# Performance work log

Hardware: AMD Instinct MI355X
Metric: run time of the kernel (lower is better)

## Reference

```python
import jax, jax.numpy as jnp
import numpy as np

B, S, D, O, E, K = 4, 1024, 512, 512, 8, 2


def setup_inputs() -> dict:
    key = jax.random.key(0)
    ks = jax.random.split(key, 9)
    sd = 1.0 / np.sqrt(D)
    so = 1.0 / np.sqrt(O)
    return {
        "x": jax.random.normal(ks[0], (B, S, D), dtype=jnp.float32),
        "gate_w": jax.random.uniform(ks[1], (D, E), minval=-sd, maxval=sd, dtype=jnp.float32),
        "gate_b": jax.random.uniform(ks[2], (E,), minval=-sd, maxval=sd, dtype=jnp.float32),
        "w1": jax.random.uniform(ks[3], (E, D, O), minval=-sd, maxval=sd, dtype=jnp.float32),
        "b1": jax.random.uniform(ks[4], (E, O), minval=-sd, maxval=sd, dtype=jnp.float32),
        "w2": jax.random.uniform(ks[5], (E, O, O), minval=-so, maxval=so, dtype=jnp.float32),
        "b2": jax.random.uniform(ks[6], (E, O), minval=-so, maxval=so, dtype=jnp.float32),
        "w3": jax.random.uniform(ks[7], (E, O, O), minval=-so, maxval=so, dtype=jnp.float32),
        "b3": jax.random.uniform(ks[8], (E, O), minval=-so, maxval=so, dtype=jnp.float32),
    }


def reference(x, gate_w, gate_b, w1, b1, w2, b2, w3, b3):
    # Gating: softmax over experts, then top-k expert selection per token.
    logits = jnp.einsum('bsd,de->bse', x, gate_w) + gate_b
    probs = jax.nn.softmax(logits, axis=-1)                 # [B,S,E]
    _, top_idx = jax.lax.top_k(probs, K)                    # [B,S,K]

    n = B * S
    xt = x.reshape(n, D)
    idx_f = top_idx.reshape(n, K)
    # Faithful quirk of the original: the combine weight for slot j is
    # gateProbabilities[b, s, j] (indexing by the SLOT index, not the
    # selected expert id), because nonzero() yields the top-k slot column.
    slot_w = probs.reshape(n, E)[:, :K]                     # [n,K]

    # Dense per-expert 3-layer MLP (grouped GEMM baseline).
    h = jax.nn.relu(jnp.einsum('nd,edh->enh', xt, w1) + b1[:, None, :])
    h = jax.nn.relu(jnp.einsum('enh,eho->eno', h, w2) + b2[:, None, :])
    y = jax.nn.relu(jnp.einsum('enh,eho->eno', h, w3) + b3[:, None, :])  # [E,n,O]

    # combine[n,e] = sum_j 1[top_idx[n,j]==e] * slot_w[n,j]
    combine = jnp.einsum('nke,nk->ne', jax.nn.one_hot(idx_f, E, dtype=xt.dtype), slot_w)
    out = jnp.einsum('ne,eno->no', combine, y)
    return out.reshape(B, S, O)
```

## Files before the change

kernel.cpp:

```cpp
#include <hip/hip_runtime.h>
#include <hip/hip_bf16.h>
#include <float.h>


#define NTOK   4096
#define DIM    512
#define NEXP   8
#define MATSZ  (DIM * DIM)

typedef _Float16 half8 __attribute__((ext_vector_type(8)));
typedef float    f32x4 __attribute__((ext_vector_type(4)));

#define META_OFF   0u
#define TOPE_OFF   1024u
#define TOPW_OFF   33792u
#define ETOK_OFF   66560u
#define EW_OFF     197632u
#define XH_OFF     328704u
#define WT_OFF     4523008u

__device__ __forceinline__ int swz(int row) {
    return ((row & 7) << 3) ^ ((row & 8) << 1);
}

__global__ __launch_bounds__(256)
void gate_kernel(const float* __restrict__ x, const float* __restrict__ gw,
                 const float* __restrict__ gb,
                 int* __restrict__ top_e, float* __restrict__ top_w,
                 _Float16* __restrict__ xh, float* __restrict__ out)
{
    int tid = threadIdx.x;
    int n = blockIdx.x * 4 + (tid >> 6);
    int lane = tid & 63;

    float4 z = {0.f, 0.f, 0.f, 0.f};
    float* op = out + (size_t)n * DIM + lane * 8;
    *(float4*)op = z;
    *(float4*)(op + 4) = z;

    const float* xr = x + (size_t)n * DIM + lane * 8;
    float4 v0 = *(const float4*)xr;
    float4 v1 = *(const float4*)(xr + 4);
    float xv[8] = {v0.x, v0.y, v0.z, v0.w, v1.x, v1.y, v1.z, v1.w};

    half8 h = { (_Float16)xv[0], (_Float16)xv[1], (_Float16)xv[2], (_Float16)xv[3],
                (_Float16)xv[4], (_Float16)xv[5], (_Float16)xv[6], (_Float16)xv[7] };
    *(half8*)(xh + (size_t)n * DIM + lane * 8) = h;

    float p[NEXP];
#pragma unroll
    for (int e = 0; e < NEXP; e++) p[e] = 0.f;
    const float* g = gw + (size_t)lane * 64;
#pragma unroll
    for (int j = 0; j < 8; j++)
#pragma unroll
        for (int e = 0; e < NEXP; e++) p[e] += xv[j] * g[j * 8 + e];
#pragma unroll
    for (int e = 0; e < NEXP; e++) {
        float v = p[e];
        for (int off = 32; off; off >>= 1) v += __shfl_xor(v, off, 64);
        p[e] = v;
    }
    if (lane == 0) {
        float l[NEXP];
#pragma unroll
        for (int e = 0; e < NEXP; e++) l[e] = p[e] + gb[e];
        float m = l[0];
#pragma unroll
        for (int e = 1; e < NEXP; e++) m = fmaxf(m, l[e]);
        float ex[NEXP], s = 0.f;
#pragma unroll
        for (int e = 0; e < NEXP; e++) { ex[e] = expf(l[e] - m); s += ex[e]; }
        int e0 = 0; float m0 = l[0];
#pragma unroll
        for (int e = 1; e < NEXP; e++) if (l[e] > m0) { m0 = l[e]; e0 = e; }
        int e1 = -1; float m1 = -FLT_MAX;
#pragma unroll
        for (int e = 0; e < NEXP; e++) if (e != e0 && l[e] > m1) { m1 = l[e]; e1 = e; }
        float inv = 1.f / s;
        top_e[2 * n + 0] = e0;
        top_e[2 * n + 1] = e1;
        top_w[2 * n + 0] = ex[0] * inv;
        top_w[2 * n + 1] = ex[1] * inv;
    }
}

__global__ __launch_bounds__(256)
void scatter_kernel(const int* __restrict__ top_e, const float* __restrict__ top_w,
                    int* __restrict__ meta, int* __restrict__ entry_tok,
                    float* __restrict__ entry_w)
{
    int n = blockIdx.x * 256 + threadIdx.x;
    int lane = threadIdx.x & 63;
#pragma unroll
    for (int j = 0; j < 2; j++) {
        int e = top_e[2 * n + j];
        float ww = top_w[2 * n + j];
        int pos = 0;
        for (int ex = 0; ex < NEXP; ex++) {
            unsigned long long m = __ballot(e == ex);
            if (e == ex) {
                int leader = __ffsll(m) - 1;
                int base = 0;
                if (lane == leader) base = atomicAdd(&meta[8 + ex], __popcll(m));
                base = __shfl(base, leader, 64);
                pos = (ex << 12) + base + __popcll(m & ((1ull << lane) - 1ull));
            }
        }
        entry_tok[pos] = n;
        entry_w[pos] = ww;
    }
}

__global__ __launch_bounds__(256)
void pack_w(const float* __restrict__ W1, const float* __restrict__ W2,
            const float* __restrict__ W3, _Float16* __restrict__ Wt)
{
    __shared__ float s[32 * 513];
    int bid = blockIdx.x;
    int mat = bid >> 4, kc = bid & 15;
    const float* src = ((mat < 8) ? W1 + (size_t)mat * MATSZ
                      : (mat < 16) ? W2 + (size_t)(mat - 8) * MATSZ
                                   : W3 + (size_t)(mat - 16) * MATSZ)
                     + (size_t)kc * 32 * DIM;
    int tid = threadIdx.x;
#pragma unroll
    for (int i = 0; i < 16; i++) {
        int idx = i * 1024 + tid * 4;
        int k = idx >> 9, c = idx & 511;
        float4 v = *(const float4*)(src + idx);
        float* d = &s[k * 513 + c];
        d[0] = v.x; d[1] = v.y; d[2] = v.z; d[3] = v.w;
    }
    __syncthreads();
    int w = tid >> 6, lane = tid & 63, l15 = lane & 15, l4 = lane >> 4;
#pragma unroll
    for (int i = 0; i < 8; i++) {
        int c16 = w * 8 + i;
        int col = c16 * 16 + l15;
        half8 h;
#pragma unroll
        for (int j = 0; j < 8; j++)
            h[j] = (_Float16)s[(l4 * 8 + j) * 513 + col];
        *(half8*)(Wt + (size_t)mat * MATSZ + (size_t)(kc * 32 + c16) * 512 + lane * 8) = h;
    }
}

__global__ __launch_bounds__(512, 2)
void fused_mlp(const _Float16* __restrict__ xh, const _Float16* __restrict__ wt,
               const float* __restrict__ b1, const float* __restrict__ b2,
               const float* __restrict__ b3, float* __restrict__ out,
               const int* __restrict__ meta, const int* __restrict__ entry_tok,
               const float* __restrict__ entry_w)
{
    __shared__ _Float16 hbuf[64 * DIM];
    __shared__ int   rtok[64];
    __shared__ float rw[64];

    int bid = blockIdx.x;
    int e = bid & 7;
    int j = bid >> 3;
    int cnt = meta[8 + e];
    if (j >= ((cnt + 63) >> 6)) return;
    int row0 = (e << 12) + (j << 6);

    int tid = threadIdx.x;
    int w = tid >> 6, l = tid & 63;
    int l15 = l & 15, l4 = l >> 4;
    int colb = w * 64 + l15;

    if (tid < 64) {
        int t = entry_tok[row0 + tid];
        rtok[tid] = t;
        rw[tid]   = entry_w[row0 + tid];
    }
    __syncthreads();

    {
        int row = tid >> 3;
        int c0 = (tid & 7) * 64;
        int tk = rtok[row]; if (tk < 0) tk = 0;
        const _Float16* src = xh + (size_t)tk * DIM + c0;
        int f = swz(row);
        _Float16* dst = hbuf + row * DIM;
#pragma unroll
        for (int q = 0; q < 8; q++) {
            half8 v = *(const half8*)(src + q * 8);
            *(half8*)(dst + ((c0 + q * 8) ^ f)) = v;
        }
    }
    __syncthreads();

    f32x4 acc[4][4];

    auto run_layer = [&](const _Float16* __restrict__ Wp) {
#pragma unroll
        for (int rg = 0; rg < 4; rg++)
#pragma unroll
            for (int cg = 0; cg < 4; cg++) acc[rg][cg] = (f32x4){0.f, 0.f, 0.f, 0.f};
        const _Float16* wb = Wp + (size_t)(w * 4) * 512 + (size_t)l * 8;
        half8 b[2][4];
#pragma unroll
        for (int cg = 0; cg < 4; cg++)
            b[0][cg] = *(const half8*)(wb + (size_t)cg * 512);
#pragma unroll
        for (int kc = 0; kc < 16; kc++) {
            const int cur = kc & 1, nxt = cur ^ 1;
            const int kn = (kc + 1) & 15;
#pragma unroll
            for (int cg = 0; cg < 4; cg++)
                b[nxt][cg] = *(const half8*)(wb + (size_t)(kn * 32 + cg) * 512);
            int koff = kc * 32 + l4 * 8;
            half8 af[4];
#pragma unroll
            for (int rg = 0; rg < 4; rg++) {
                int row = rg * 16 + l15;
                af[rg] = *(const half8*)(hbuf + row * DIM + (koff ^ swz(row)));
            }
#pragma unroll
            for (int rg = 0; rg < 4; rg++)
#pragma unroll
                for (int cg = 0; cg < 4; cg++)
                    acc[rg][cg] = __builtin_amdgcn_mfma_f32_16x16x32_f16(af[rg], b[cur][cg], acc[rg][cg], 0, 0, 0);
        }
    };

    auto writeback = [&](const float* __restrict__ Bias) {
        float bs[4];
#pragma unroll
        for (int cg = 0; cg < 4; cg++) bs[cg] = Bias[e * DIM + colb + cg * 16];
        __syncthreads();
#pragma unroll
        for (int rg = 0; rg < 4; rg++)
#pragma unroll
            for (int r = 0; r < 4; r++) {
                int row = rg * 16 + l4 * 4 + r;
                int f = swz(row);
                _Float16* dst = hbuf + row * DIM;
#pragma unroll
                for (int cg = 0; cg < 4; cg++)
                    dst[(colb + cg * 16) ^ f] = (_Float16)fmaxf(acc[rg][cg][r] + bs[cg], 0.f);
            }
        __syncthreads();
    };

    run_layer(wt + (size_t)e * MATSZ);        writeback(b1);
    run_layer(wt + (size_t)(8 + e) * MATSZ);  writeback(b2);
    run_layer(wt + (size_t)(16 + e) * MATSZ);

    float bs[4];
#pragma unroll
    for (int cg = 0; cg < 4; cg++) bs[cg] = b3[e * DIM + colb + cg * 16];
#pragma unroll
    for (int rg = 0; rg < 4; rg++)
#pragma unroll
        for (int r = 0; r < 4; r++) {
            int row = rg * 16 + l4 * 4 + r;
            int tok = rtok[row];
            if (tok >= 0) {
                float ww = rw[row];
                float* op = out + (size_t)tok * DIM + colb;
#pragma unroll
                for (int cg = 0; cg < 4; cg++) {
                    float v = fmaxf(acc[rg][cg][r] + bs[cg], 0.f);
                    atomicAdd(op + cg * 16, ww * v);
                }
            }
        }
}

extern "C" void kernel_launch(void* const* d_in, const int* in_sizes, int n_in,
                              void* d_out, int out_size, void* d_ws, size_t ws_size,
                              hipStream_t stream)
{
    const float* x      = (const float*)d_in[0];
    const float* gate_w = (const float*)d_in[1];
    const float* gate_b = (const float*)d_in[2];
    const float* w1     = (const float*)d_in[3];
    const float* b1     = (const float*)d_in[4];
    const float* w2     = (const float*)d_in[5];
    const float* b2     = (const float*)d_in[6];
    const float* w3     = (const float*)d_in[7];
    const float* b3     = (const float*)d_in[8];
    float* out = (float*)d_out;

    char* ws = (char*)d_ws;
    int*      meta      = (int*)(ws + META_OFF);
    int*      top_e     = (int*)(ws + TOPE_OFF);
    float*    top_w     = (float*)(ws + TOPW_OFF);
    int*      entry_tok = (int*)(ws + ETOK_OFF);
    float*    entry_w   = (float*)(ws + EW_OFF);
    _Float16* xh        = (_Float16*)(ws + XH_OFF);
    _Float16* wt        = (_Float16*)(ws + WT_OFF);

    hipMemsetAsync(meta, 0, 256, stream);

    gate_kernel<<<NTOK / 4, 256, 0, stream>>>(x, gate_w, gate_b, top_e, top_w, xh, out);
    scatter_kernel<<<NTOK / 256, 256, 0, stream>>>(top_e, top_w, meta, entry_tok, entry_w);
    pack_w<<<24 * 16, 256, 0, stream>>>(w1, w2, w3, wt);

    fused_mlp<<<NEXP * 64, 512, 0, stream>>>(xh, wt, b1, b2, b3, out,
                                             meta, entry_tok, entry_w);
}
```

Measured before the change: 158.5 us.

## Replace atomic combine with slot buffer plus gather kernel, merge gate and weight pack

Merges the weight-pack and gating kernels into one launch. Rewrites scatter to use block-local shared-memory counters and padded global counters, and records each token's slot positions. The MLP kernel now writes unweighted expert outputs to a slot buffer instead of doing float atomicAdds into the output, and a new combine kernel gathers and weights the two slots per token. The B-fragment prefetch is deepened to three buffers and the MFMA block is wrapped in raised wave priority. This adds an extra kernel and an intermediate buffer round trip in exchange for removing atomics and the output zeroing.

```diff
diff --git a/kernel.cpp b/kernel.cpp
--- a/kernel.cpp
+++ b/kernel.cpp
@@ -14,29 +14,59 @@
 #define META_OFF   0u
 #define TOPE_OFF   1024u
 #define TOPW_OFF   33792u
-#define ETOK_OFF   66560u
-#define EW_OFF     197632u
-#define XH_OFF     328704u
-#define WT_OFF     4523008u
+#define INV_OFF    66560u
+#define ETOK_OFF   99328u
+#define XH_OFF     230400u
+#define WT_OFF     4424704u
+#define Y_OFF      17007616u
 
 __device__ __forceinline__ int swz(int row) {
     return ((row & 7) << 3) ^ ((row & 8) << 1);
 }
 
 __global__ __launch_bounds__(256)
-void gate_kernel(const float* __restrict__ x, const float* __restrict__ gw,
+void prep_kernel(const float* __restrict__ x, const float* __restrict__ gw,
                  const float* __restrict__ gb,
+                 const float* __restrict__ W1, const float* __restrict__ W2,
+                 const float* __restrict__ W3,
                  int* __restrict__ top_e, float* __restrict__ top_w,
-                 _Float16* __restrict__ xh, float* __restrict__ out)
-{
+                 _Float16* __restrict__ xh, _Float16* __restrict__ Wt)
+{
+    __shared__ float s[32 * 513];
+    int bid = blockIdx.x;
     int tid = threadIdx.x;
-    int n = blockIdx.x * 4 + (tid >> 6);
+
+    if (bid < 384) {
+        int mat = bid >> 4, kc = bid & 15;
+        const float* src = ((mat < 8) ? W1 + (size_t)mat * MATSZ
+                          : (mat < 16) ? W2 + (size_t)(mat - 8) * MATSZ
+                                       : W3 + (size_t)(mat - 16) * MATSZ)
+                         + (size_t)kc * 32 * DIM;
+#pragma unroll
+        for (int i = 0; i < 16; i++) {
+            int idx = i * 1024 + tid * 4;
+            int k = idx >> 9, c = idx & 511;
+            float4 v = *(const float4*)(src + idx);
+            float* d = &s[k * 513 + c];
+            d[0] = v.x; d[1] = v.y; d[2] = v.z; d[3] = v.w;
+        }
+        __syncthreads();
+        int w = tid >> 6, lane = tid & 63, l15 = lane & 15, l4 = lane >> 4;
+#pragma unroll
+        for (int i = 0; i < 8; i++) {
+            int c16 = w * 8 + i;
+            int col = c16 * 16 + l15;
+            half8 h;
+#pragma unroll
+            for (int j = 0; j < 8; j++)
+                h[j] = (_Float16)s[(l4 * 8 + j) * 513 + col];
+            *(half8*)(Wt + (size_t)mat * MATSZ + (size_t)(kc * 32 + c16) * 512 + lane * 8) = h;
+        }
+        return;
+    }
+
+    int n = (bid - 384) * 4 + (tid >> 6);
     int lane = tid & 63;
-
-    float4 z = {0.f, 0.f, 0.f, 0.f};
-    float* op = out + (size_t)n * DIM + lane * 8;
-    *(float4*)op = z;
-    *(float4*)(op + 4) = z;
 
     const float* xr = x + (size_t)n * DIM + lane * 8;
     float4 v0 = *(const float4*)xr;
@@ -68,99 +98,63 @@
         float m = l[0];
 #pragma unroll
         for (int e = 1; e < NEXP; e++) m = fmaxf(m, l[e]);
-        float ex[NEXP], s = 0.f;
-#pragma unroll
-        for (int e = 0; e < NEXP; e++) { ex[e] = expf(l[e] - m); s += ex[e]; }
+        float ex[NEXP], sum = 0.f;
+#pragma unroll
+        for (int e = 0; e < NEXP; e++) { ex[e] = expf(l[e] - m); sum += ex[e]; }
         int e0 = 0; float m0 = l[0];
 #pragma unroll
         for (int e = 1; e < NEXP; e++) if (l[e] > m0) { m0 = l[e]; e0 = e; }
         int e1 = -1; float m1 = -FLT_MAX;
 #pragma unroll
         for (int e = 0; e < NEXP; e++) if (e != e0 && l[e] > m1) { m1 = l[e]; e1 = e; }
-        float inv = 1.f / s;
-        top_e[2 * n + 0] = e0;
-        top_e[2 * n + 1] = e1;
-        top_w[2 * n + 0] = ex[0] * inv;
-        top_w[2 * n + 1] = ex[1] * inv;
+        float inv = 1.f / sum;
+        int2 te = {e0, e1};
+        *(int2*)(top_e + 2 * n) = te;
+        float2 tw = {ex[0] * inv, ex[1] * inv};
+        *(float2*)(top_w + 2 * n) = tw;
     }
 }
 
 __global__ __launch_bounds__(256)
-void scatter_kernel(const int* __restrict__ top_e, const float* __restrict__ top_w,
-                    int* __restrict__ meta, int* __restrict__ entry_tok,
-                    float* __restrict__ entry_w)
-{
-    int n = blockIdx.x * 256 + threadIdx.x;
-    int lane = threadIdx.x & 63;
-#pragma unroll
-    for (int j = 0; j < 2; j++) {
-        int e = top_e[2 * n + j];
-        float ww = top_w[2 * n + j];
-        int pos = 0;
-        for (int ex = 0; ex < NEXP; ex++) {
-            unsigned long long m = __ballot(e == ex);
-            if (e == ex) {
-                int leader = __ffsll(m) - 1;
-                int base = 0;
-                if (lane == leader) base = atomicAdd(&meta[8 + ex], __popcll(m));
-                base = __shfl(base, leader, 64);
-                pos = (ex << 12) + base + __popcll(m & ((1ull << lane) - 1ull));
-            }
-        }
-        entry_tok[pos] = n;
-        entry_w[pos] = ww;
-    }
-}
-
-__global__ __launch_bounds__(256)
-void pack_w(const float* __restrict__ W1, const float* __restrict__ W2,
-            const float* __restrict__ W3, _Float16* __restrict__ Wt)
-{
-    __shared__ float s[32 * 513];
-    int bid = blockIdx.x;
-    int mat = bid >> 4, kc = bid & 15;
-    const float* src = ((mat < 8) ? W1 + (size_t)mat * MATSZ
-                      : (mat < 16) ? W2 + (size_t)(mat - 8) * MATSZ
-                                   : W3 + (size_t)(mat - 16) * MATSZ)
-                     + (size_t)kc * 32 * DIM;
+void scatter_kernel(const int* __restrict__ top_e, int* __restrict__ meta,
+                    int* __restrict__ entry_tok, int* __restrict__ inv_pos)
+{
+    __shared__ int lcnt[NEXP];
+    __shared__ int lbase[NEXP];
     int tid = threadIdx.x;
-#pragma unroll
-    for (int i = 0; i < 16; i++) {
-        int idx = i * 1024 + tid * 4;
-        int k = idx >> 9, c = idx & 511;
-        float4 v = *(const float4*)(src + idx);
-        float* d = &s[k * 513 + c];
-        d[0] = v.x; d[1] = v.y; d[2] = v.z; d[3] = v.w;
-    }
-    __syncthreads();
-    int w = tid >> 6, lane = tid & 63, l15 = lane & 15, l4 = lane >> 4;
-#pragma unroll
-    for (int i = 0; i < 8; i++) {
-        int c16 = w * 8 + i;
-        int col = c16 * 16 + l15;
-        half8 h;
-#pragma unroll
-        for (int j = 0; j < 8; j++)
-            h[j] = (_Float16)s[(l4 * 8 + j) * 513 + col];
-        *(half8*)(Wt + (size_t)mat * MATSZ + (size_t)(kc * 32 + c16) * 512 + lane * 8) = h;
-    }
+    if (tid < NEXP) lcnt[tid] = 0;
+    __syncthreads();
+
+    int n = blockIdx.x * 256 + tid;
+    int2 ee = *(const int2*)(top_e + 2 * n);
+    int r0 = atomicAdd(&lcnt[ee.x], 1);
+    int r1 = atomicAdd(&lcnt[ee.y], 1);
+    __syncthreads();
+
+    if (tid < NEXP) lbase[tid] = atomicAdd(&meta[tid * 16], lcnt[tid]);
+    __syncthreads();
+
+    int p0 = (ee.x << 12) + lbase[ee.x] + r0;
+    int p1 = (ee.y << 12) + lbase[ee.y] + r1;
+    entry_tok[p0] = n;
+    entry_tok[p1] = n;
+    int2 pp = {p0, p1};
+    *(int2*)(inv_pos + 2 * n) = pp;
 }
 
 __global__ __launch_bounds__(512, 2)
 void fused_mlp(const _Float16* __restrict__ xh, const _Float16* __restrict__ wt,
                const float* __restrict__ b1, const float* __restrict__ b2,
-               const float* __restrict__ b3, float* __restrict__ out,
-               const int* __restrict__ meta, const int* __restrict__ entry_tok,
-               const float* __restrict__ entry_w)
+               const float* __restrict__ b3, float* __restrict__ y,
+               const int* __restrict__ meta, const int* __restrict__ entry_tok)
 {
     __shared__ _Float16 hbuf[64 * DIM];
-    __shared__ int   rtok[64];
-    __shared__ float rw[64];
+    __shared__ int rtok[64];
 
     int bid = blockIdx.x;
     int e = bid & 7;
     int j = bid >> 3;
-    int cnt = meta[8 + e];
+    int cnt = meta[e * 16];
     if (j >= ((cnt + 63) >> 6)) return;
     int row0 = (e << 12) + (j << 6);
 
@@ -169,11 +163,8 @@
     int l15 = l & 15, l4 = l >> 4;
     int colb = w * 64 + l15;
 
-    if (tid < 64) {
-        int t = entry_tok[row0 + tid];
-        rtok[tid] = t;
-        rw[tid]   = entry_w[row0 + tid];
-    }
+    if (tid < 64)
+        rtok[tid] = entry_tok[row0 + tid];
     __syncthreads();
 
     {
@@ -199,17 +190,20 @@
 #pragma unroll
             for (int cg = 0; cg < 4; cg++) acc[rg][cg] = (f32x4){0.f, 0.f, 0.f, 0.f};
         const _Float16* wb = Wp + (size_t)(w * 4) * 512 + (size_t)l * 8;
-        half8 b[2][4];
-#pragma unroll
-        for (int cg = 0; cg < 4; cg++)
-            b[0][cg] = *(const half8*)(wb + (size_t)cg * 512);
+        half8 b[3][4];
+#pragma unroll
+        for (int cg = 0; cg < 4; cg++) {
+            b[0][cg] = *(const half8*)(wb + (size_t)(0 * 32 + cg) * 512);
+            b[1][cg] = *(const half8*)(wb + (size_t)(1 * 32 + cg) * 512);
+        }
 #pragma unroll
         for (int kc = 0; kc < 16; kc++) {
-            const int cur = kc & 1, nxt = cur ^ 1;
-            const int kn = (kc + 1) & 15;
+            const int cur = kc % 3;
+            const int pf  = (kc + 2) % 3;
+            const int kn  = (kc + 2) & 15;
 #pragma unroll
             for (int cg = 0; cg < 4; cg++)
-                b[nxt][cg] = *(const half8*)(wb + (size_t)(kn * 32 + cg) * 512);
+                b[pf][cg] = *(const half8*)(wb + (size_t)(kn * 32 + cg) * 512);
             int koff = kc * 32 + l4 * 8;
             half8 af[4];
 #pragma unroll
@@ -217,11 +211,13 @@
                 int row = rg * 16 + l15;
                 af[rg] = *(const half8*)(hbuf + row * DIM + (koff ^ swz(row)));
             }
+            __builtin_amdgcn_s_setprio(1);
 #pragma unroll
             for (int rg = 0; rg < 4; rg++)
 #pragma unroll
                 for (int cg = 0; cg < 4; cg++)
                     acc[rg][cg] = __builtin_amdgcn_mfma_f32_16x16x32_f16(af[rg], b[cur][cg], acc[rg][cg], 0, 0, 0);
+            __builtin_amdgcn_s_setprio(0);
         }
     };
 
@@ -251,22 +247,46 @@
     float bs[4];
 #pragma unroll
     for (int cg = 0; cg < 4; cg++) bs[cg] = b3[e * DIM + colb + cg * 16];
+    float* yb = y + (size_t)row0 * DIM;
 #pragma unroll
     for (int rg = 0; rg < 4; rg++)
 #pragma unroll
         for (int r = 0; r < 4; r++) {
             int row = rg * 16 + l4 * 4 + r;
-            int tok = rtok[row];
-            if (tok >= 0) {
-                float ww = rw[row];
-                float* op = out + (size_t)tok * DIM + colb;
-#pragma unroll
-                for (int cg = 0; cg < 4; cg++) {
-                    float v = fmaxf(acc[rg][cg][r] + bs[cg], 0.f);
-                    atomicAdd(op + cg * 16, ww * v);
-                }
-            }
-        }
+            float* yp = yb + (size_t)row * DIM + colb;
+#pragma unroll
+            for (int cg = 0; cg < 4; cg++)
+                yp[cg * 16] = fmaxf(acc[rg][cg][r] + bs[cg], 0.f);
+        }
+}
+
+__global__ __launch_bounds__(256)
+void combine_kernel(const float* __restrict__ y, const int* __restrict__ inv_pos,
+                    const float* __restrict__ top_w, float* __restrict__ out)
+{
+    int tid = threadIdx.x;
+    int n = blockIdx.x * 4 + (tid >> 6);
+    int lane = tid & 63;
+    int2 pp = *(const int2*)(inv_pos + 2 * n);
+    float2 tw = *(const float2*)(top_w + 2 * n);
+    const float* y0 = y + (size_t)pp.x * DIM + lane * 8;
+    const float* y1 = y + (size_t)pp.y * DIM + lane * 8;
+    float4 a0 = *(const float4*)y0;
+    float4 a1 = *(const float4*)(y0 + 4);
+    float4 c0 = *(const float4*)y1;
+    float4 c1 = *(const float4*)(y1 + 4);
+    float4 o0, o1;
+    o0.x = tw.x * a0.x + tw.y * c0.x;
+    o0.y = tw.x * a0.y + tw.y * c0.y;
+    o0.z = tw.x * a0.z + tw.y * c0.z;
+    o0.w = tw.x * a0.w + tw.y * c0.w;
+    o1.x = tw.x * a1.x + tw.y * c1.x;
+    o1.y = tw.x * a1.y + tw.y * c1.y;
+    o1.z = tw.x * a1.z + tw.y * c1.z;
+    o1.w = tw.x * a1.w + tw.y * c1.w;
+    float* op = out + (size_t)n * DIM + lane * 8;
+    *(float4*)op = o0;
+    *(float4*)(op + 4) = o1;
 }
 
 extern "C" void kernel_launch(void* const* d_in, const int* in_sizes, int n_in,
@@ -288,17 +308,18 @@
     int*      meta      = (int*)(ws + META_OFF);
     int*      top_e     = (int*)(ws + TOPE_OFF);
     float*    top_w     = (float*)(ws + TOPW_OFF);
+    int*      inv_pos   = (int*)(ws + INV_OFF);
     int*      entry_tok = (int*)(ws + ETOK_OFF);
-    float*    entry_w   = (float*)(ws + EW_OFF);
     _Float16* xh        = (_Float16*)(ws + XH_OFF);
     _Float16* wt        = (_Float16*)(ws + WT_OFF);
-
-    hipMemsetAsync(meta, 0, 256, stream);
-
-    gate_kernel<<<NTOK / 4, 256, 0, stream>>>(x, gate_w, gate_b, top_e, top_w, xh, out);
-    scatter_kernel<<<NTOK / 256, 256, 0, stream>>>(top_e, top_w, meta, entry_tok, entry_w);
-    pack_w<<<24 * 16, 256, 0, stream>>>(w1, w2, w3, wt);
-
-    fused_mlp<<<NEXP * 64, 512, 0, stream>>>(xh, wt, b1, b2, b3, out,
-                                             meta, entry_tok, entry_w);
-}
+    float*    yslot     = (float*)(ws + Y_OFF);
+
+    hipMemsetAsync(meta, 0, 1024, stream);
+
+    prep_kernel<<<384 + NTOK / 4, 256, 0, stream>>>(x, gate_w, gate_b, w1, w2, w3,
+                                                    top_e, top_w, xh, wt);
+    scatter_kernel<<<NTOK / 256, 256, 0, stream>>>(top_e, meta, entry_tok, inv_pos);
+    fused_mlp<<<NEXP * 64, 512, 0, stream>>>(xh, wt, b1, b2, b3, yslot,
+                                             meta, entry_tok);
+    combine_kernel<<<NTOK / 4, 256, 0, stream>>>(yslot, inv_pos, top_w, out);
+}
```

Measured after the change: 135.5 us. 1.17x faster.
